# Performance work log

Measured on AMD Instinct MI355X. Metric: run time of the kernel, lower is better.

## Reference

```python
import jax, jax.numpy as jnp
import numpy as np

B, N, D = 4, 2048, 1024
H, HD = 16, 64
MAX_SEQ = 4096
INNER = H * HD


def setup_inputs() -> dict:
    key = jax.random.key(0)
    ks = jax.random.split(key, 5)
    s = 0.02
    return {
        "x": jax.random.normal(ks[0], (B, N, D), dtype=jnp.float32),
        "ln_gamma": jnp.ones((D,), jnp.float32),
        "ln_beta": jnp.zeros((D,), jnp.float32),
        "w_qkv": jax.random.normal(ks[1], (D, 3 * INNER), dtype=jnp.float32) * s,
        "w_out": jax.random.normal(ks[2], (INNER, D), dtype=jnp.float32) * s,
        "b_out": jnp.zeros((D,), jnp.float32),
    }


def _rope_tables(n, head_dim):
    inv_freq = 1.0 / (10000.0 ** (jnp.arange(0, head_dim, 2, dtype=jnp.float32) / head_dim))
    pos = jnp.arange(n, dtype=jnp.float32)
    ang = pos[:, None] * inv_freq[None, :]  # [n, hd/2]
    return jnp.sin(ang), jnp.cos(ang)


def reference(x, ln_gamma, ln_beta, w_qkv, w_out, b_out):
    b, n, d = x.shape
    # LayerNorm
    mu = jnp.mean(x, axis=-1, keepdims=True)
    var = jnp.var(x, axis=-1, keepdims=True)
    xn = (x - mu) / jnp.sqrt(var + 1e-5) * ln_gamma + ln_beta
    # QKV projection (no bias)
    qkv = xn @ w_qkv  # [b, n, 3*inner]
    q, k, v = jnp.split(qkv, 3, axis=-1)
    def to_heads(t):
        return t.reshape(b, n, H, HD).transpose(0, 2, 1, 3)  # b h n d
    q, k, v = to_heads(q), to_heads(k), to_heads(v)
    # RoPE (half-split rotation, as in source)
    sin, cos = _rope_tables(n, HD)  # [n, hd/2]
    sin = sin[None, None]
    cos = cos[None, None]
    half = HD // 2
    def rotate(t):
        t1, t2 = t[..., :half], t[..., half:]
        return jnp.concatenate([t1 * cos - t2 * sin, t2 * cos + t1 * sin], axis=-1)
    qr, kr = rotate(q), rotate(k)
    scale = HD ** -0.5
    scores = jnp.einsum('bhid,bhjd->bhij', qr, kr) * scale
    probs = jax.nn.softmax(scores, axis=-1)
    out = jnp.einsum('bhij,bhjd->bhid', probs, v)
    out = out.transpose(0, 2, 1, 3).reshape(b, n, INNER)
    return out @ w_out + b_out
```

## Files before the change

### kernel.cpp

```cpp
#include <hip/hip_runtime.h>
#include <hip/hip_bf16.h>

#define Bb   4
#define Nn   2048
#define Dd   1024
#define Hh   16
#define HDd  64
#define IN3  3072
#define RR   8192

typedef __attribute__((ext_vector_type(8))) short short8;
typedef __attribute__((ext_vector_type(4))) float floatx4;

#define MFMA16(a, b, c) __builtin_amdgcn_mfma_f32_16x16x32_bf16((a), (b), (c), 0, 0, 0)

static __device__ __forceinline__ unsigned short f2bf(float f) {
    union { float f; unsigned int u; } v; v.f = f;
    unsigned int r = v.u + 0x7fffu + ((v.u >> 16) & 1u);
    return (unsigned short)(r >> 16);
}
static __device__ __forceinline__ float bf2f(unsigned short h) {
    union { unsigned int u; float f; } v; v.u = ((unsigned int)h) << 16;
    return v.f;
}

static __device__ __forceinline__ float fast_exp2(float x) {
#if __has_builtin(__builtin_amdgcn_exp2f)
    return __builtin_amdgcn_exp2f(x);
#else
    return exp2f(x);
#endif
}

static __device__ __forceinline__ void sincos_rev(float ang, float& s, float& c) {
#if __has_builtin(__builtin_amdgcn_sinf) && __has_builtin(__builtin_amdgcn_cosf)
    float rev = ang * 0.15915494309189535f;
    rev = rev - floorf(rev);
    s = __builtin_amdgcn_sinf(rev);
    c = __builtin_amdgcn_cosf(rev);
#else
    s = sinf(ang);
    c = cosf(ang);
#endif
}

typedef const __attribute__((address_space(1))) void* gas1_t;
typedef __attribute__((address_space(3))) void* las3_t;
static __device__ __forceinline__ void load_lds16(const void* g, void* l) {
    __builtin_amdgcn_global_load_lds((gas1_t)(unsigned long long)g,
                                     (las3_t)(unsigned int)(unsigned long long)l,
                                     16, 0, 0);
}

__global__ void transpose_w(const float* __restrict__ src, unsigned short* __restrict__ dst,
                            int rows, int cols) {
    __shared__ float tile[32][33];
    int c0 = blockIdx.x * 32, r0 = blockIdx.y * 32;
    int tx = threadIdx.x, ty = threadIdx.y;
#pragma unroll
    for (int i = 0; i < 4; ++i) tile[ty + 8 * i][tx] = src[(r0 + ty + 8 * i) * cols + c0 + tx];
    __syncthreads();
#pragma unroll
    for (int i = 0; i < 4; ++i) dst[(c0 + ty + 8 * i) * rows + r0 + tx] = f2bf(tile[tx][ty + 8 * i]);
}

__global__ __launch_bounds__(256) void ln_kernel(const float* __restrict__ x,
                                                 const float* __restrict__ g,
                                                 const float* __restrict__ be,
                                                 unsigned short* __restrict__ xn) {
    int row = blockIdx.x, t = threadIdx.x;
    float4 v = ((const float4*)(x + row * Dd))[t];
    float s  = v.x + v.y + v.z + v.w;
    float sq = v.x * v.x + v.y * v.y + v.z * v.z + v.w * v.w;
#pragma unroll
    for (int off = 1; off < 64; off <<= 1) { s += __shfl_xor(s, off); sq += __shfl_xor(sq, off); }
    __shared__ float ps[4], pq2[4];
    int wv = t >> 6;
    if ((t & 63) == 0) { ps[wv] = s; pq2[wv] = sq; }
    __syncthreads();
    s  = ps[0] + ps[1] + ps[2] + ps[3];
    sq = pq2[0] + pq2[1] + pq2[2] + pq2[3];
    float mu   = s * (1.0f / Dd);
    float var  = sq * (1.0f / Dd) - mu * mu;
    float rstd = rsqrtf(var + 1e-5f);
    float4 gg = ((const float4*)g)[t];
    float4 bb = ((const float4*)be)[t];
    ushort4 o;
    o.x = f2bf((v.x - mu) * rstd * gg.x + bb.x);
    o.y = f2bf((v.y - mu) * rstd * gg.y + bb.y);
    o.z = f2bf((v.z - mu) * rstd * gg.z + bb.z);
    o.w = f2bf((v.w - mu) * rstd * gg.w + bb.w);
    ((ushort4*)(xn + row * Dd))[t] = o;
}

__global__ __launch_bounds__(512, 1) void gemm_qkv(const unsigned short* __restrict__ A,
                                                   const unsigned short* __restrict__ Bt,
                                                   unsigned short* __restrict__ qo,
                                                   unsigned short* __restrict__ ko,
                                                   unsigned short* __restrict__ vo) {
    __shared__ unsigned short LDS[49152];
    int r0 = blockIdx.x * 128, c0 = blockIdx.y * 256;
    int tid = threadIdx.x;
    int wv = tid >> 6, lane = tid & 63, l15 = lane & 15, quad = lane >> 4;
    int wm = wv >> 2, wn = wv & 3;

    floatx4 acc[4][4] = {};
    int swz0 = (quad ^ (l15 & 7)) << 3;
    int swz1 = ((4 | quad) ^ (l15 & 7)) << 3;

    auto stageA = [&](int tt) {
        unsigned short* base = &LDS[(tt & 1) * 8192];
        int k0 = tt * 64;
#pragma unroll
        for (int i = 0; i < 2; ++i) {
            int qq = (wv * 2 + i) * 64 + lane;
            int row = qq >> 3, cp = qq & 7;
            int sc = cp ^ (row & 7);
            load_lds16(&A[(r0 + row) * 1024 + k0 + sc * 8], &base[qq * 8]);
        }
    };
    auto stageB = [&](int tt) {
        unsigned short* base = &LDS[16384 + (tt & 1) * 16384];
        int k0 = tt * 64;
#pragma unroll
        for (int i = 0; i < 4; ++i) {
            int qq = (wv * 4 + i) * 64 + lane;
            int row = qq >> 3, cp = qq & 7;
            int sc = cp ^ (row & 7);
            load_lds16(&Bt[(c0 + row) * 1024 + k0 + sc * 8], &base[qq * 8]);
        }
    };

    stageA(0); stageB(0); stageA(1);
    asm volatile("s_waitcnt vmcnt(2)" ::: "memory");
    __builtin_amdgcn_s_barrier();

    for (int t = 0; t < 16; ++t) {
        int abuf = (t & 1) * 8192;
        int bbuf = 16384 + (t & 1) * 16384;
        short8 af[4][2], bf[2][2];

        if (t < 15) stageB(t + 1);
#pragma unroll
        for (int mi = 0; mi < 4; ++mi) {
            af[mi][0] = *(const short8*)&LDS[abuf + (wm * 64 + mi * 16 + l15) * 64 + swz0];
            af[mi][1] = *(const short8*)&LDS[abuf + (wm * 64 + mi * 16 + l15) * 64 + swz1];
        }
#pragma unroll
        for (int ni = 0; ni < 2; ++ni) {
            bf[ni][0] = *(const short8*)&LDS[bbuf + (wn * 64 + ni * 16 + l15) * 64 + swz0];
            bf[ni][1] = *(const short8*)&LDS[bbuf + (wn * 64 + ni * 16 + l15) * 64 + swz1];
        }
        __builtin_amdgcn_s_barrier();
        asm volatile("s_waitcnt lgkmcnt(0)" ::: "memory");
        __builtin_amdgcn_s_setprio(1);
#pragma unroll
        for (int ks = 0; ks < 2; ++ks)
#pragma unroll
            for (int mi = 0; mi < 4; ++mi)
#pragma unroll
                for (int ni = 0; ni < 2; ++ni)
                    acc[mi][ni] = MFMA16(af[mi][ks], bf[ni][ks], acc[mi][ni]);
        __builtin_amdgcn_s_setprio(0);
        __builtin_amdgcn_s_barrier();

        if (t < 14) stageA(t + 2);
#pragma unroll
        for (int ni = 0; ni < 2; ++ni) {
            bf[ni][0] = *(const short8*)&LDS[bbuf + (wn * 64 + 32 + ni * 16 + l15) * 64 + swz0];
            bf[ni][1] = *(const short8*)&LDS[bbuf + (wn * 64 + 32 + ni * 16 + l15) * 64 + swz1];
        }
        __builtin_amdgcn_s_barrier();
        asm volatile("s_waitcnt lgkmcnt(0)" ::: "memory");
        __builtin_amdgcn_s_setprio(1);
#pragma unroll
        for (int ks = 0; ks < 2; ++ks)
#pragma unroll
            for (int mi = 0; mi < 4; ++mi)
#pragma unroll
                for (int ni = 0; ni < 2; ++ni)
                    acc[mi][2 + ni] = MFMA16(af[mi][ks], bf[ni][ks], acc[mi][2 + ni]);
        __builtin_amdgcn_s_setprio(0);
        if (t < 14)       asm volatile("s_waitcnt vmcnt(2)" ::: "memory");
        else if (t == 14) asm volatile("s_waitcnt vmcnt(0)" ::: "memory");
        __builtin_amdgcn_s_barrier();
    }

    if (c0 < 2048) {
        const float crope = 13.287712379549449f / 32.0f;
        float invf0 = fast_exp2(-(float)l15 * crope);
        float invf1 = fast_exp2(-(float)(l15 + 16) * crope);
#pragma unroll
        for (int mi = 0; mi < 4; ++mi)
#pragma unroll
            for (int r2 = 0; r2 < 4; ++r2) {
                int rr = r0 + wm * 64 + mi * 16 + quad * 4 + r2;
                float n = (float)(rr & 2047);
                float s0, c0r, s1, c1r;
                sincos_rev(n * invf0, s0, c0r);
                sincos_rev(n * invf1, s1, c1r);
                float t1a = acc[mi][0][r2], t2a = acc[mi][2][r2];
                acc[mi][0][r2] = t1a * c0r - t2a * s0;
                acc[mi][2][r2] = t2a * c0r + t1a * s0;
                float t1b = acc[mi][1][r2], t2b = acc[mi][3][r2];
                acc[mi][1][r2] = t1b * c1r - t2b * s1;
                acc[mi][3][r2] = t2b * c1r + t1b * s1;
            }
    }
    if (c0 < 1024) {
        const float qsc = 0.125f * 1.4426950408889634f;
#pragma unroll
        for (int mi = 0; mi < 4; ++mi)
#pragma unroll
            for (int ni = 0; ni < 4; ++ni)
#pragma unroll
                for (int r2 = 0; r2 < 4; ++r2) acc[mi][ni][r2] *= qsc;
    }
    unsigned short* outp = (c0 < 1024) ? qo : (c0 < 2048) ? ko : vo;
#pragma unroll
    for (int ni = 0; ni < 4; ++ni) {
        int c = c0 + wn * 64 + ni * 16 + l15;
        int cin = c & 1023;
        int h = cin >> 6, j = cin & 63;
#pragma unroll
        for (int mi = 0; mi < 4; ++mi) {
#pragma unroll
            for (int r2 = 0; r2 < 4; ++r2) {
                int rr = r0 + wm * 64 + mi * 16 + quad * 4 + r2;
                int b = rr >> 11, n = rr & 2047;
                int bh = b * 16 + h;
                outp[(bh * 2048 + n) * 64 + j] = f2bf(acc[mi][ni][r2]);
            }
        }
    }
}

__global__ __launch_bounds__(256) void vtrans(const unsigned short* __restrict__ v,
                                              unsigned short* __restrict__ vt) {
    __shared__ unsigned short T[64][72];
    int bh = blockIdx.y, n0 = blockIdx.x * 64;
    int t = threadIdx.x;
    int nl = t >> 2, c = (t & 3) * 16;
    const unsigned short* src = v + ((bh * 2048) + n0 + nl) * 64 + c;
    *(short8*)&T[nl][c]     = *(const short8*)src;
    *(short8*)&T[nl][c + 8] = *(const short8*)(src + 8);
    __syncthreads();
    int hd = t >> 2, nc = (t & 3) * 16;
    unsigned short tmp[16];
#pragma unroll
    for (int i = 0; i < 16; ++i) {
        int pos = nc + i;
        int blk = pos >> 5, p = pos & 31;
        int kq = (p >> 3) & 3, hh = (p >> 2) & 1, r = p & 3;
        tmp[i] = T[blk * 32 + hh * 16 + kq * 4 + r][hd];
    }
    unsigned short* dst = vt + ((bh * 64) + hd) * 2048 + n0 + nc;
    *(short8*)dst       = *(const short8*)&tmp[0];
    *(short8*)(dst + 8) = *(const short8*)&tmp[8];
}

__global__ __launch_bounds__(256, 3) void attn_kernel(const unsigned short* __restrict__ q,
                                                      const unsigned short* __restrict__ k,
                                                      const unsigned short* __restrict__ vt,
                                                      unsigned short* __restrict__ attn) {
    __shared__ unsigned short KVs[3][2][64 * 64];
    int fid = blockIdx.x;
    int xcd = fid & 7, rest = fid >> 3;
    int qi = rest & 15, bhg = rest >> 4;
    int bh = bhg * 8 + xcd;
    int q0 = qi * 128;
    int tid = threadIdx.x;
    int wave = tid >> 6, lane = tid & 63, l15 = lane & 15, quad = lane >> 4;
    const unsigned short* qb  = q  + bh * (Nn * HDd);
    const unsigned short* kbp = k  + bh * (Nn * HDd);
    const unsigned short* vb  = vt + bh * (HDd * Nn);
    int qbase = q0 + wave * 32;

    short8 bq[2][2];
#pragma unroll
    for (int g = 0; g < 2; ++g) {
        bq[g][0] = *(const short8*)&qb[(qbase + g * 16 + l15) * 64 + quad * 8];
        bq[g][1] = *(const short8*)&qb[(qbase + g * 16 + l15) * 64 + 32 + quad * 8];
    }

    auto stage = [&](int buf, int kb0) {
#pragma unroll
        for (int i = 0; i < 2; ++i) {
            int c = wave * 2 + i;
            int p = c * 64 + lane;
            int row = p >> 3, pr = p & 7;
            int sc = pr ^ (row & 7);
            load_lds16(&kbp[(kb0 + row) * 64 + sc * 8], &KVs[buf][0][p * 8]);
            load_lds16(&vb[row * Nn + kb0 + sc * 8],    &KVs[buf][1][p * 8]);
        }
    };

    floatx4 ot[2][4] = {};
    floatx4 osum[2] = {};
    const floatx4 fz = {0.0f, 0.0f, 0.0f, 0.0f};
    const short8 vones = {(short)0x3F80, (short)0x3F80, (short)0x3F80, (short)0x3F80,
                          (short)0x3F80, (short)0x3F80, (short)0x3F80, (short)0x3F80};
    int swz0 = (quad ^ (l15 & 7)) << 3;
    int swz1 = ((4 | quad) ^ (l15 & 7)) << 3;

    auto body = [&](int cur, int nxt, int kt) {
        if (kt + 2 < 32) stage(nxt, (kt + 2) * 64);
        const unsigned short* Kc = KVs[cur][0];
        const unsigned short* Vc = KVs[cur][1];
        short8 ka0[4], ka1[4];
#pragma unroll
        for (int mb = 0; mb < 4; ++mb) {
            ka0[mb] = *(const short8*)&Kc[(mb * 16 + l15) * 64 + swz0];
            ka1[mb] = *(const short8*)&Kc[(mb * 16 + l15) * 64 + swz1];
        }
        short8 bv0[4], bv1[4];
#pragma unroll
        for (int ht = 0; ht < 4; ++ht) {
            int row = (ht * 16 + l15) * 64;
            bv0[ht] = *(const short8*)&Vc[row + swz0];
            bv1[ht] = *(const short8*)&Vc[row + swz1];
        }
#pragma unroll
        for (int g = 0; g < 2; ++g) {
            floatx4 st[4];
            __builtin_amdgcn_s_setprio(1);
#pragma unroll
            for (int mb = 0; mb < 4; ++mb) {
                floatx4 z = MFMA16(ka0[mb], bq[g][0], fz);
                st[mb] = MFMA16(ka1[mb], bq[g][1], z);
            }
            __builtin_amdgcn_s_setprio(0);
            short8 pa[2];
#pragma unroll
            for (int c = 0; c < 2; ++c) {
                union { ushort4 u[2]; short8 s; } w;
#pragma unroll
                for (int t2 = 0; t2 < 2; ++t2) {
                    int mb = 2 * c + t2;
                    float p0 = fast_exp2(st[mb][0]);
                    float p1 = fast_exp2(st[mb][1]);
                    float p2 = fast_exp2(st[mb][2]);
                    float p3 = fast_exp2(st[mb][3]);
                    *(__hip_bfloat162*)&w.u[t2].x = __float22bfloat162_rn(float2{p0, p1});
                    *(__hip_bfloat162*)&w.u[t2].z = __float22bfloat162_rn(float2{p2, p3});
                }
                pa[c] = w.s;
            }
            __builtin_amdgcn_s_setprio(1);
            osum[g] = MFMA16(pa[0], vones, osum[g]);
            osum[g] = MFMA16(pa[1], vones, osum[g]);
#pragma unroll
            for (int ht = 0; ht < 4; ++ht) {
                ot[g][ht] = MFMA16(pa[0], bv0[ht], ot[g][ht]);
                ot[g][ht] = MFMA16(pa[1], bv1[ht], ot[g][ht]);
            }
            __builtin_amdgcn_s_setprio(0);
        }
        if (kt < 30)       asm volatile("s_waitcnt vmcnt(4)" ::: "memory");
        else if (kt == 30) asm volatile("s_waitcnt vmcnt(0)" ::: "memory");
        __builtin_amdgcn_s_barrier();
    };

    stage(0, 0);
    stage(1, 64);
    asm volatile("s_waitcnt vmcnt(4)" ::: "memory");
    __builtin_amdgcn_s_barrier();
    for (int kt = 0; kt < 30; kt += 3) {
        body(0, 2, kt);
        body(1, 0, kt + 1);
        body(2, 1, kt + 2);
    }
    body(0, 2, 30);
    body(1, 0, 31);

    int b = bh >> 4, h = bh & 15;
    unsigned short* ob = ((unsigned short*)KVs) + wave * 1152;
#pragma unroll
    for (int g = 0; g < 2; ++g) {
        float il[4];
#pragma unroll
        for (int r = 0; r < 4; ++r) il[r] = 1.0f / osum[g][r];
#pragma unroll
        for (int ht = 0; ht < 4; ++ht)
#pragma unroll
            for (int r = 0; r < 4; ++r)
                ob[(quad * 4 + r) * 72 + ht * 16 + l15] = f2bf(ot[g][ht][r] * il[r]);
        int q_loc = lane >> 2, seg = lane & 3;
        unsigned short* dst = attn + ((long)(b * Nn + q0 + wave * 32 + g * 16 + q_loc)) * 1024 + h * 64 + seg * 16;
        *(short8*)dst       = *(const short8*)&ob[q_loc * 72 + seg * 16];
        *(short8*)(dst + 8) = *(const short8*)&ob[q_loc * 72 + seg * 16 + 8];
    }
}

__global__ __launch_bounds__(256) void gemm_out(const unsigned short* __restrict__ A,
                                                const unsigned short* __restrict__ Bt,
                                                const float* __restrict__ bout,
                                                float* __restrict__ out) {
    __shared__ unsigned short As[128 * 64];
    __shared__ unsigned short Bs[128 * 64];
    int r0 = blockIdx.x * 128, c0 = blockIdx.y * 128;
    int tid = threadIdx.x;
    int wave = tid >> 6, lane = tid & 63, l15 = lane & 15, quad = lane >> 4;
    int wm = wave & 1, wn = wave >> 1;
    floatx4 acc[4][4] = {};
    int swz0 = (quad ^ (l15 & 7)) << 3;
    int swz1 = ((4 | quad) ^ (l15 & 7)) << 3;
    for (int k0 = 0; k0 < 1024; k0 += 64) {
#pragma unroll
        for (int i = 0; i < 4; ++i) {
            int c = wave * 4 + i;
            int p = c * 64 + lane;
            int row = p >> 3, pr = p & 7;
            int sc = pr ^ (row & 7);
            load_lds16(&A[(r0 + row) * 1024 + k0 + sc * 8],  &As[p * 8]);
            load_lds16(&Bt[(c0 + row) * 1024 + k0 + sc * 8], &Bs[p * 8]);
        }
        __syncthreads();
#pragma unroll
        for (int ks = 0; ks < 2; ++ks) {
            int sw = ks ? swz1 : swz0;
            short8 af[4], bf[4];
#pragma unroll
            for (int mi = 0; mi < 4; ++mi)
                af[mi] = *(const short8*)&As[(wm * 64 + mi * 16 + l15) * 64 + sw];
#pragma unroll
            for (int ni = 0; ni < 4; ++ni)
                bf[ni] = *(const short8*)&Bs[(wn * 64 + ni * 16 + l15) * 64 + sw];
#pragma unroll
            for (int mi = 0; mi < 4; ++mi)
#pragma unroll
                for (int ni = 0; ni < 4; ++ni)
                    acc[mi][ni] = MFMA16(af[mi], bf[ni], acc[mi][ni]);
        }
        __syncthreads();
    }
#pragma unroll
    for (int ni = 0; ni < 4; ++ni) {
        int c = c0 + wn * 64 + ni * 16 + l15;
        float bias = bout[c];
#pragma unroll
        for (int mi = 0; mi < 4; ++mi)
#pragma unroll
            for (int r2 = 0; r2 < 4; ++r2) {
                int rr = r0 + wm * 64 + mi * 16 + quad * 4 + r2;
                out[rr * 1024 + c] = acc[mi][ni][r2] + bias;
            }
    }
}

extern "C" void kernel_launch(void* const* d_in, const int* in_sizes, int n_in,
                              void* d_out, int out_size, void* d_ws, size_t ws_size,
                              hipStream_t stream) {
    const float* x    = (const float*)d_in[0];
    const float* g    = (const float*)d_in[1];
    const float* be   = (const float*)d_in[2];
    const float* wqkv = (const float*)d_in[3];
    const float* wout = (const float*)d_in[4];
    const float* bout = (const float*)d_in[5];
    float* out = (float*)d_out;

    char* ws = (char*)d_ws;
    unsigned short* xn    = (unsigned short*)(ws);
    unsigned short* wqkvT = (unsigned short*)(ws + 16777216);
    unsigned short* woutT = (unsigned short*)(ws + 23068672);
    unsigned short* qb    = (unsigned short*)(ws + 25165824);
    unsigned short* kb    = (unsigned short*)(ws + 41943040);
    unsigned short* vt    = (unsigned short*)(ws + 58720256);
    unsigned short* attn  = (unsigned short*)(ws + 75497472);
    unsigned short* vtmp  = attn;

    transpose_w<<<dim3(IN3 / 32, Dd / 32), dim3(32, 8), 0, stream>>>(wqkv, wqkvT, Dd, IN3);
    transpose_w<<<dim3(Dd / 32, Dd / 32), dim3(32, 8), 0, stream>>>(wout, woutT, Dd, Dd);
    ln_kernel<<<RR, 256, 0, stream>>>(x, g, be, xn);
    gemm_qkv<<<dim3(RR / 128, IN3 / 256), 512, 0, stream>>>(xn, wqkvT, qb, kb, vtmp);
    vtrans<<<dim3(Nn / 64, Bb * Hh), 256, 0, stream>>>(vtmp, vt);
    attn_kernel<<<dim3(Nn / 128 * Bb * Hh), 256, 0, stream>>>(qb, kb, vt, attn);
    gemm_out<<<dim3(RR / 128, Dd / 128), 256, 0, stream>>>(attn, woutT, bout, out);
}
```

Before: 268.9 us.

## Rewrite output GEMM as pipelined 128x256 tile and double-buffer attention

The output projection GEMM moves to 512-thread blocks with 128x256 tiles. It double-buffers A and B tiles in LDS and issues global-to-LDS prefetches in the middle of the MFMA phases, so memory latency overlaps compute instead of hitting a barrier every K step. The attention kernel drops from a triple-buffered to a double-buffered K/V ring, which cuts its LDS use so a fourth block can fit per CU. The trade-off is less prefetch depth in attention, since each step now waits on vmcnt(0), and fewer blocks in the output GEMM grid.

```diff
diff --git a/kernel.cpp b/kernel.cpp
--- a/kernel.cpp
+++ b/kernel.cpp
@@ -259,11 +259,11 @@
     *(short8*)(dst + 8) = *(const short8*)&tmp[8];
 }
 
-__global__ __launch_bounds__(256, 3) void attn_kernel(const unsigned short* __restrict__ q,
+__global__ __launch_bounds__(256, 4) void attn_kernel(const unsigned short* __restrict__ q,
                                                       const unsigned short* __restrict__ k,
                                                       const unsigned short* __restrict__ vt,
                                                       unsigned short* __restrict__ attn) {
-    __shared__ unsigned short KVs[3][2][64 * 64];
+    __shared__ unsigned short KVs[2][2][64 * 64];
     int fid = blockIdx.x;
     int xcd = fid & 7, rest = fid >> 3;
     int qi = rest & 15, bhg = rest >> 4;
@@ -303,8 +303,8 @@
     int swz0 = (quad ^ (l15 & 7)) << 3;
     int swz1 = ((4 | quad) ^ (l15 & 7)) << 3;
 
-    auto body = [&](int cur, int nxt, int kt) {
-        if (kt + 2 < 32) stage(nxt, (kt + 2) * 64);
+    auto body = [&](int cur, int kt) {
+        if (kt < 31) stage(cur ^ 1, (kt + 1) * 64);
         const unsigned short* Kc = KVs[cur][0];
         const unsigned short* Vc = KVs[cur][1];
         short8 ka0[4], ka1[4];
@@ -356,22 +356,17 @@
             }
             __builtin_amdgcn_s_setprio(0);
         }
-        if (kt < 30)       asm volatile("s_waitcnt vmcnt(4)" ::: "memory");
-        else if (kt == 30) asm volatile("s_waitcnt vmcnt(0)" ::: "memory");
+        if (kt < 31) asm volatile("s_waitcnt vmcnt(0)" ::: "memory");
         __builtin_amdgcn_s_barrier();
     };
 
     stage(0, 0);
-    stage(1, 64);
-    asm volatile("s_waitcnt vmcnt(4)" ::: "memory");
+    asm volatile("s_waitcnt vmcnt(0)" ::: "memory");
     __builtin_amdgcn_s_barrier();
-    for (int kt = 0; kt < 30; kt += 3) {
-        body(0, 2, kt);
-        body(1, 0, kt + 1);
-        body(2, 1, kt + 2);
-    }
-    body(0, 2, 30);
-    body(1, 0, 31);
+    for (int kt = 0; kt < 32; kt += 2) {
+        body(0, kt);
+        body(1, kt + 1);
+    }
 
     int b = bh >> 4, h = bh & 15;
     unsigned short* ob = ((unsigned short*)KVs) + wave * 1152;
@@ -392,48 +387,98 @@
     }
 }
 
-__global__ __launch_bounds__(256) void gemm_out(const unsigned short* __restrict__ A,
-                                                const unsigned short* __restrict__ Bt,
-                                                const float* __restrict__ bout,
-                                                float* __restrict__ out) {
-    __shared__ unsigned short As[128 * 64];
-    __shared__ unsigned short Bs[128 * 64];
-    int r0 = blockIdx.x * 128, c0 = blockIdx.y * 128;
+__global__ __launch_bounds__(512, 1) void gemm_out(const unsigned short* __restrict__ A,
+                                                   const unsigned short* __restrict__ Bt,
+                                                   const float* __restrict__ bout,
+                                                   float* __restrict__ out) {
+    __shared__ unsigned short LDS[49152];
+    int r0 = blockIdx.x * 128, c0 = blockIdx.y * 256;
     int tid = threadIdx.x;
-    int wave = tid >> 6, lane = tid & 63, l15 = lane & 15, quad = lane >> 4;
-    int wm = wave & 1, wn = wave >> 1;
+    int wv = tid >> 6, lane = tid & 63, l15 = lane & 15, quad = lane >> 4;
+    int wm = wv >> 2, wn = wv & 3;
+
     floatx4 acc[4][4] = {};
     int swz0 = (quad ^ (l15 & 7)) << 3;
     int swz1 = ((4 | quad) ^ (l15 & 7)) << 3;
-    for (int k0 = 0; k0 < 1024; k0 += 64) {
+
+    auto stageA = [&](int tt) {
+        unsigned short* base = &LDS[(tt & 1) * 8192];
+        int k0 = tt * 64;
+#pragma unroll
+        for (int i = 0; i < 2; ++i) {
+            int qq = (wv * 2 + i) * 64 + lane;
+            int row = qq >> 3, cp = qq & 7;
+            int sc = cp ^ (row & 7);
+            load_lds16(&A[(r0 + row) * 1024 + k0 + sc * 8], &base[qq * 8]);
+        }
+    };
+    auto stageB = [&](int tt) {
+        unsigned short* base = &LDS[16384 + (tt & 1) * 16384];
+        int k0 = tt * 64;
 #pragma unroll
         for (int i = 0; i < 4; ++i) {
-            int c = wave * 4 + i;
-            int p = c * 64 + lane;
-            int row = p >> 3, pr = p & 7;
-            int sc = pr ^ (row & 7);
-            load_lds16(&A[(r0 + row) * 1024 + k0 + sc * 8],  &As[p * 8]);
-            load_lds16(&Bt[(c0 + row) * 1024 + k0 + sc * 8], &Bs[p * 8]);
-        }
-        __syncthreads();
-#pragma unroll
-        for (int ks = 0; ks < 2; ++ks) {
-            int sw = ks ? swz1 : swz0;
-            short8 af[4], bf[4];
+            int qq = (wv * 4 + i) * 64 + lane;
+            int row = qq >> 3, cp = qq & 7;
+            int sc = cp ^ (row & 7);
+            load_lds16(&Bt[(c0 + row) * 1024 + k0 + sc * 8], &base[qq * 8]);
+        }
+    };
+
+    stageA(0); stageB(0); stageA(1);
+    asm volatile("s_waitcnt vmcnt(2)" ::: "memory");
+    __builtin_amdgcn_s_barrier();
+
+    for (int t = 0; t < 16; ++t) {
+        int abuf = (t & 1) * 8192;
+        int bbuf = 16384 + (t & 1) * 16384;
+        short8 af[4][2], bf[2][2];
+
+        if (t < 15) stageB(t + 1);
+#pragma unroll
+        for (int mi = 0; mi < 4; ++mi) {
+            af[mi][0] = *(const short8*)&LDS[abuf + (wm * 64 + mi * 16 + l15) * 64 + swz0];
+            af[mi][1] = *(const short8*)&LDS[abuf + (wm * 64 + mi * 16 + l15) * 64 + swz1];
+        }
+#pragma unroll
+        for (int ni = 0; ni < 2; ++ni) {
+            bf[ni][0] = *(const short8*)&LDS[bbuf + (wn * 64 + ni * 16 + l15) * 64 + swz0];
+            bf[ni][1] = *(const short8*)&LDS[bbuf + (wn * 64 + ni * 16 + l15) * 64 + swz1];
+        }
+        __builtin_amdgcn_s_barrier();
+        asm volatile("s_waitcnt lgkmcnt(0)" ::: "memory");
+        __builtin_amdgcn_s_setprio(1);
+#pragma unroll
+        for (int ks = 0; ks < 2; ++ks)
 #pragma unroll
             for (int mi = 0; mi < 4; ++mi)
-                af[mi] = *(const short8*)&As[(wm * 64 + mi * 16 + l15) * 64 + sw];
-#pragma unroll
-            for (int ni = 0; ni < 4; ++ni)
-                bf[ni] = *(const short8*)&Bs[(wn * 64 + ni * 16 + l15) * 64 + sw];
+#pragma unroll
+                for (int ni = 0; ni < 2; ++ni)
+                    acc[mi][ni] = MFMA16(af[mi][ks], bf[ni][ks], acc[mi][ni]);
+        __builtin_amdgcn_s_setprio(0);
+        __builtin_amdgcn_s_barrier();
+
+        if (t < 14) stageA(t + 2);
+#pragma unroll
+        for (int ni = 0; ni < 2; ++ni) {
+            bf[ni][0] = *(const short8*)&LDS[bbuf + (wn * 64 + 32 + ni * 16 + l15) * 64 + swz0];
+            bf[ni][1] = *(const short8*)&LDS[bbuf + (wn * 64 + 32 + ni * 16 + l15) * 64 + swz1];
+        }
+        __builtin_amdgcn_s_barrier();
+        asm volatile("s_waitcnt lgkmcnt(0)" ::: "memory");
+        __builtin_amdgcn_s_setprio(1);
+#pragma unroll
+        for (int ks = 0; ks < 2; ++ks)
 #pragma unroll
             for (int mi = 0; mi < 4; ++mi)
 #pragma unroll
-                for (int ni = 0; ni < 4; ++ni)
-                    acc[mi][ni] = MFMA16(af[mi], bf[ni], acc[mi][ni]);
-        }
-        __syncthreads();
-    }
+                for (int ni = 0; ni < 2; ++ni)
+                    acc[mi][2 + ni] = MFMA16(af[mi][ks], bf[ni][ks], acc[mi][2 + ni]);
+        __builtin_amdgcn_s_setprio(0);
+        if (t < 14)       asm volatile("s_waitcnt vmcnt(2)" ::: "memory");
+        else if (t == 14) asm volatile("s_waitcnt vmcnt(0)" ::: "memory");
+        __builtin_amdgcn_s_barrier();
+    }
+
 #pragma unroll
     for (int ni = 0; ni < 4; ++ni) {
         int c = c0 + wn * 64 + ni * 16 + l15;
@@ -475,5 +520,5 @@
     gemm_qkv<<<dim3(RR / 128, IN3 / 256), 512, 0, stream>>>(xn, wqkvT, qb, kb, vtmp);
     vtrans<<<dim3(Nn / 64, Bb * Hh), 256, 0, stream>>>(vtmp, vt);
     attn_kernel<<<dim3(Nn / 128 * Bb * Hh), 256, 0, stream>>>(qb, kb, vt, attn);
-    gemm_out<<<dim3(RR / 128, Dd / 128), 256, 0, stream>>>(attn, woutT, bout, out);
-}
+    gemm_out<<<dim3(RR / 128, Dd / 256), 512, 0, stream>>>(attn, woutT, bout, out);
+}
```

Result: slower. 529.0 us (+96.7%).
